# Kernel optimization log

Measured on AMD Instinct MI355X. Metric: run time of the kernel, lower is better.

Reference implementation:

```python
import jax, jax.numpy as jnp
import numpy as np

B, S1, S2, H, H2, D, K = 1, 1024, 8192, 32, 8, 128, 128


def setup_inputs() -> dict:
    key = jax.random.key(0)
    k1, k2, k3, k4 = jax.random.split(key, 4)
    q = jax.random.normal(k1, (B, S1, H, D), dtype=jnp.float16)
    k = jax.random.normal(k2, (B, S2, H2, D), dtype=jnp.float16)
    v = jax.random.normal(k3, (B, S2, H2, D), dtype=jnp.float16)
    sparse_indices = jax.random.randint(k4, (B, S1, H2, K), 0, S2, dtype=jnp.int32)
    return {"q": q, "k": k, "v": v, "sparse_indices": sparse_indices}


def reference(q, k, v, sparse_indices):
    # q: [B,S1,H,D]  k,v: [B,S2,H2,D]  sparse_indices: [B,S1,H2,K]
    b, s1, h, d = q.shape
    h2 = sparse_indices.shape[2]
    g = h // h2  # GQA group size
    scale = 1.0 / np.sqrt(d).astype(np.float32)
    qg = q.reshape(b, s1, h2, g, d)  # group queries per kv head
    b_idx = jnp.arange(b)[:, None, None, None]
    h_idx = jnp.arange(h2)[None, None, :, None]
    # gather per-query sparse KV sets: [B,S1,H2,K,D]
    kg = k[b_idx, sparse_indices, h_idx]
    vg = v[b_idx, sparse_indices, h_idx]
    scores = jnp.einsum('bshgd,bshkd->bshgk', qg, kg).astype(jnp.float32) * scale
    p = jax.nn.softmax(scores, axis=-1).astype(q.dtype)
    out = jnp.einsum('bshgk,bshkd->bshgd', p, vg)  # [B,S1,H2,G,D]
    return out.reshape(b, s1, h, d).astype(jnp.float16)
```

## Files before the change

kernel.cpp:

```cpp
#include <hip/hip_runtime.h>
#include <stdint.h>
#include <math.h>

#define NH 32
#define NH2 8
#define DD 128
#define KSEL 128
#define GG 4
#define S2MASK 8191
#define KVELTS (8192 * NH2 * DD)

typedef _Float16 h8   __attribute__((ext_vector_type(8)));
typedef _Float16 h2t  __attribute__((ext_vector_type(2)));
typedef __fp16   hp2  __attribute__((ext_vector_type(2)));
typedef float    f32x4 __attribute__((ext_vector_type(4)));

static __device__ __forceinline__ h8 cvt8(float4 a, float4 b) {
  union { h8 v; hp2 p[4]; } u;
  u.p[0] = __builtin_amdgcn_cvt_pkrtz(a.x, a.y);
  u.p[1] = __builtin_amdgcn_cvt_pkrtz(a.z, a.w);
  u.p[2] = __builtin_amdgcn_cvt_pkrtz(b.x, b.y);
  u.p[3] = __builtin_amdgcn_cvt_pkrtz(b.z, b.w);
  return u.v;
}

__global__ __launch_bounds__(256) void convert_kv(
    const float4* __restrict__ kf, const float4* __restrict__ vf,
    ushort4* __restrict__ kh, ushort4* __restrict__ vh, int n4) {
  int i = blockIdx.x * blockDim.x + threadIdx.x;
  const int stride = gridDim.x * blockDim.x;
  union { ushort4 u; hp2 p[2]; } ua;
  for (; i < n4; i += stride) {
    float4 a = kf[i];
    ua.p[0] = __builtin_amdgcn_cvt_pkrtz(a.x, a.y);
    ua.p[1] = __builtin_amdgcn_cvt_pkrtz(a.z, a.w);
    kh[i] = ua.u;
    float4 b = vf[i];
    ua.p[0] = __builtin_amdgcn_cvt_pkrtz(b.x, b.y);
    ua.p[1] = __builtin_amdgcn_cvt_pkrtz(b.z, b.w);
    vh[i] = ua.u;
  }
}

#define WAVE_FENCE() asm volatile("" ::: "memory")

__global__ __launch_bounds__(256) void sparse_attn_f16(
    const float* __restrict__ q, const _Float16* __restrict__ kh,
    const _Float16* __restrict__ vh, const int* __restrict__ idx,
    float* __restrict__ out) {
  __shared__ int sOff[4][KSEL];
  __shared__ __align__(16) float sP[4][KSEL][GG];

  const int tid = threadIdx.x;
  const int w = tid >> 6;
  const int lane = tid & 63;
  const int h2 = blockIdx.x & 7;
  const int s1 = ((blockIdx.x >> 3) << 2) + w;

  const int* ip = idx + (s1 * NH2 + h2) * KSEL;
  sOff[w][lane]      = (ip[lane]      & S2MASK) * (NH2 * DD);
  sOff[w][lane + 64] = (ip[lane + 64] & S2MASK) * (NH2 * DD);

  const int m  = lane & 15;
  const int kg = lane >> 4;

  h8 aq[4];
#pragma unroll
  for (int t = 0; t < 4; ++t)
#pragma unroll
    for (int i = 0; i < 8; ++i) aq[t][i] = (_Float16)0;
  if (m < GG) {
    const float* qp = q + (s1 * NH + h2 * GG + m) * DD + kg * 8;
#pragma unroll
    for (int t = 0; t < 4; ++t) {
      float4 f0 = *(const float4*)(qp + 32 * t);
      float4 f1 = *(const float4*)(qp + 32 * t + 4);
      aq[t] = cvt8(f0, f1);
    }
  }

  WAVE_FENCE();

  const float scale = 0.08838834764831845f;

#pragma unroll 2
  for (int nt = 0; nt < 8; ++nt) {
    const _Float16* kp = kh + sOff[w][nt * 16 + m] + h2 * DD + kg * 8;
    f32x4 acc = {0.f, 0.f, 0.f, 0.f};
#pragma unroll
    for (int t = 0; t < 4; ++t) {
      h8 bk = *(const h8*)(kp + 32 * t);
      acc = __builtin_amdgcn_mfma_f32_16x16x32_f16(aq[t], bk, acc, 0, 0, 0);
    }
    if (lane < 16) {
      float4 sc = make_float4(acc[0] * scale, acc[1] * scale,
                              acc[2] * scale, acc[3] * scale);
      *(float4*)&sP[w][nt * 16 + lane][0] = sc;
    }
  }

  WAVE_FENCE();

  {
    float4 p0 = *(const float4*)&sP[w][lane][0];
    float4 p1 = *(const float4*)&sP[w][lane + 64][0];
    float4 mx = make_float4(fmaxf(p0.x, p1.x), fmaxf(p0.y, p1.y),
                            fmaxf(p0.z, p1.z), fmaxf(p0.w, p1.w));
#pragma unroll
    for (int off = 1; off < 64; off <<= 1) {
      mx.x = fmaxf(mx.x, __shfl_xor(mx.x, off));
      mx.y = fmaxf(mx.y, __shfl_xor(mx.y, off));
      mx.z = fmaxf(mx.z, __shfl_xor(mx.z, off));
      mx.w = fmaxf(mx.w, __shfl_xor(mx.w, off));
    }
    float4 e0 = make_float4(__expf(p0.x - mx.x), __expf(p0.y - mx.y),
                            __expf(p0.z - mx.z), __expf(p0.w - mx.w));
    float4 e1 = make_float4(__expf(p1.x - mx.x), __expf(p1.y - mx.y),
                            __expf(p1.z - mx.z), __expf(p1.w - mx.w));
    float4 sm = make_float4(e0.x + e1.x, e0.y + e1.y, e0.z + e1.z, e0.w + e1.w);
#pragma unroll
    for (int off = 1; off < 64; off <<= 1) {
      sm.x += __shfl_xor(sm.x, off);
      sm.y += __shfl_xor(sm.y, off);
      sm.z += __shfl_xor(sm.z, off);
      sm.w += __shfl_xor(sm.w, off);
    }
    float4 inv = make_float4(1.f / fmaxf(sm.x, 1e-30f), 1.f / fmaxf(sm.y, 1e-30f),
                             1.f / fmaxf(sm.z, 1e-30f), 1.f / fmaxf(sm.w, 1e-30f));
    *(float4*)&sP[w][lane][0] =
        make_float4(e0.x * inv.x, e0.y * inv.y, e0.z * inv.z, e0.w * inv.w);
    *(float4*)&sP[w][lane + 64][0] =
        make_float4(e1.x * inv.x, e1.y * inv.y, e1.z * inv.z, e1.w * inv.w);
  }

  WAVE_FENCE();

  float a00 = 0.f, a01 = 0.f, a10 = 0.f, a11 = 0.f;
  float a20 = 0.f, a21 = 0.f, a30 = 0.f, a31 = 0.f;
  const _Float16* vb = vh + h2 * DD + lane * 2;
#pragma unroll
  for (int ch = 0; ch < 8; ++ch) {
    h2t vv[16];
#pragma unroll
    for (int j = 0; j < 16; ++j)
      vv[j] = *(const h2t*)(vb + sOff[w][ch * 16 + j]);
#pragma unroll
    for (int j = 0; j < 16; ++j) {
      const float4 p = *(const float4*)&sP[w][ch * 16 + j][0];
      const float vx = (float)vv[j][0];
      const float vy = (float)vv[j][1];
      a00 = fmaf(p.x, vx, a00); a01 = fmaf(p.x, vy, a01);
      a10 = fmaf(p.y, vx, a10); a11 = fmaf(p.y, vy, a11);
      a20 = fmaf(p.z, vx, a20); a21 = fmaf(p.z, vy, a21);
      a30 = fmaf(p.w, vx, a30); a31 = fmaf(p.w, vy, a31);
    }
  }

  float* op = out + (s1 * NH + h2 * GG) * DD + lane * 2;
  *(float2*)(op + 0 * DD) = make_float2(a00, a01);
  *(float2*)(op + 1 * DD) = make_float2(a10, a11);
  *(float2*)(op + 2 * DD) = make_float2(a20, a21);
  *(float2*)(op + 3 * DD) = make_float2(a30, a31);
}

__global__ __launch_bounds__(256) void sparse_attn_f32(
    const float* __restrict__ q, const float* __restrict__ k,
    const float* __restrict__ v, const int* __restrict__ idx,
    float* __restrict__ out) {
  __shared__ int sIdx[4][KSEL];
  __shared__ __align__(16) float sP[4][KSEL][GG];

  const int tid = threadIdx.x;
  const int w = tid >> 6;
  const int lane = tid & 63;
  const int h2 = blockIdx.x & 7;
  const int s1 = ((blockIdx.x >> 3) << 2) + w;

  const int* ip = idx + (s1 * NH2 + h2) * KSEL;
  sIdx[w][lane]      = ip[lane] & S2MASK;
  sIdx[w][lane + 64] = ip[lane + 64] & S2MASK;

  const int m  = lane & 15;
  const int kg = lane >> 4;

  h8 aq[4];
#pragma unroll
  for (int t = 0; t < 4; ++t)
#pragma unroll
    for (int i = 0; i < 8; ++i) aq[t][i] = (_Float16)0;
  if (m < GG) {
    const float* qp = q + (s1 * NH + h2 * GG + m) * DD + kg * 8;
#pragma unroll
    for (int t = 0; t < 4; ++t) {
      float4 f0 = *(const float4*)(qp + 32 * t);
      float4 f1 = *(const float4*)(qp + 32 * t + 4);
      aq[t] = cvt8(f0, f1);
    }
  }
  __syncthreads();

  const float scale = 0.08838834764831845f;
#pragma unroll 2
  for (int nt = 0; nt < 8; ++nt) {
    const int s2 = sIdx[w][nt * 16 + m];
    const float* kp = k + (s2 * NH2 + h2) * DD + kg * 8;
    f32x4 acc = {0.f, 0.f, 0.f, 0.f};
#pragma unroll
    for (int t = 0; t < 4; ++t) {
      float4 f0 = *(const float4*)(kp + 32 * t);
      float4 f1 = *(const float4*)(kp + 32 * t + 4);
      acc = __builtin_amdgcn_mfma_f32_16x16x32_f16(aq[t], cvt8(f0, f1), acc, 0, 0, 0);
    }
    if (lane < 16) {
      float4 sc = make_float4(acc[0] * scale, acc[1] * scale,
                              acc[2] * scale, acc[3] * scale);
      *(float4*)&sP[w][nt * 16 + lane][0] = sc;
    }
  }
  __syncthreads();

  {
    float4 p0 = *(const float4*)&sP[w][lane][0];
    float4 p1 = *(const float4*)&sP[w][lane + 64][0];
    float4 mx = make_float4(fmaxf(p0.x, p1.x), fmaxf(p0.y, p1.y),
                            fmaxf(p0.z, p1.z), fmaxf(p0.w, p1.w));
#pragma unroll
    for (int off = 1; off < 64; off <<= 1) {
      mx.x = fmaxf(mx.x, __shfl_xor(mx.x, off));
      mx.y = fmaxf(mx.y, __shfl_xor(mx.y, off));
      mx.z = fmaxf(mx.z, __shfl_xor(mx.z, off));
      mx.w = fmaxf(mx.w, __shfl_xor(mx.w, off));
    }
    float4 e0 = make_float4(__expf(p0.x - mx.x), __expf(p0.y - mx.y),
                            __expf(p0.z - mx.z), __expf(p0.w - mx.w));
    float4 e1 = make_float4(__expf(p1.x - mx.x), __expf(p1.y - mx.y),
                            __expf(p1.z - mx.z), __expf(p1.w - mx.w));
    float4 sm = make_float4(e0.x + e1.x, e0.y + e1.y, e0.z + e1.z, e0.w + e1.w);
#pragma unroll
    for (int off = 1; off < 64; off <<= 1) {
      sm.x += __shfl_xor(sm.x, off);
      sm.y += __shfl_xor(sm.y, off);
      sm.z += __shfl_xor(sm.z, off);
      sm.w += __shfl_xor(sm.w, off);
    }
    float4 inv = make_float4(1.f / fmaxf(sm.x, 1e-30f), 1.f / fmaxf(sm.y, 1e-30f),
                             1.f / fmaxf(sm.z, 1e-30f), 1.f / fmaxf(sm.w, 1e-30f));
    *(float4*)&sP[w][lane][0] =
        make_float4(e0.x * inv.x, e0.y * inv.y, e0.z * inv.z, e0.w * inv.w);
    *(float4*)&sP[w][lane + 64][0] =
        make_float4(e1.x * inv.x, e1.y * inv.y, e1.z * inv.z, e1.w * inv.w);
  }
  __syncthreads();

  float a00 = 0.f, a01 = 0.f, a10 = 0.f, a11 = 0.f;
  float a20 = 0.f, a21 = 0.f, a30 = 0.f, a31 = 0.f;
  const float* vb = v + h2 * DD + lane * 2;
#pragma unroll 8
  for (int j = 0; j < KSEL; ++j) {
    const int s2 = sIdx[w][j];
    const float2 vv = *(const float2*)(vb + (size_t)s2 * (NH2 * DD));
    const float4 p = *(const float4*)&sP[w][j][0];
    a00 = fmaf(p.x, vv.x, a00); a01 = fmaf(p.x, vv.y, a01);
    a10 = fmaf(p.y, vv.x, a10); a11 = fmaf(p.y, vv.y, a11);
    a20 = fmaf(p.z, vv.x, a20); a21 = fmaf(p.z, vv.y, a21);
    a30 = fmaf(p.w, vv.x, a30); a31 = fmaf(p.w, vv.y, a31);
  }

  float* op = out + (s1 * NH + h2 * GG) * DD + lane * 2;
  *(float2*)(op + 0 * DD) = make_float2(a00, a01);
  *(float2*)(op + 1 * DD) = make_float2(a10, a11);
  *(float2*)(op + 2 * DD) = make_float2(a20, a21);
  *(float2*)(op + 3 * DD) = make_float2(a30, a31);
}

extern "C" void kernel_launch(void* const* d_in, const int* in_sizes, int n_in,
                              void* d_out, int out_size, void* d_ws, size_t ws_size,
                              hipStream_t stream) {
  const float* q = (const float*)d_in[0];
  const float* k = (const float*)d_in[1];
  const float* v = (const float*)d_in[2];
  const int* idx = (const int*)d_in[3];
  float* out = (float*)d_out;

  const size_t need = (size_t)2 * KVELTS * sizeof(_Float16);
  if (ws_size >= need) {
    _Float16* kh = (_Float16*)d_ws;
    _Float16* vh = kh + KVELTS;
    convert_kv<<<dim3(2048), dim3(256), 0, stream>>>(
        (const float4*)k, (const float4*)v,
        (ushort4*)kh, (ushort4*)vh, KVELTS / 4);
    sparse_attn_f16<<<dim3(2048), dim3(256), 0, stream>>>(q, kh, vh, idx, out);
  } else {
    sparse_attn_f32<<<dim3(2048), dim3(256), 0, stream>>>(q, k, v, idx, out);
  }
}
```

Measured before the change: 167.8 us.

## Stage sparse V rows into LDS with async global_load_lds prefetch

V rows gathered by sparse index now go into a per-wave LDS buffer using direct global-to-LDS loads of 16 bytes each, eight rows at a time. The first chunk is issued before the QK phase and the next chunk is prefetched while the current one is consumed. The aim is to replace the many scattered 4-byte per-lane V loads with fully coalesced 256-byte row loads and to overlap that traffic with compute. With a single buffer, each chunk must be read into registers and drained before the next load overwrites it, so explicit waitcnt and sched barriers serialize the steps and limit how much overlap is possible.

```diff
diff --git a/kernel.cpp b/kernel.cpp
--- a/kernel.cpp
+++ b/kernel.cpp
@@ -9,11 +9,20 @@
 #define GG 4
 #define S2MASK 8191
 #define KVELTS (8192 * NH2 * DD)
+#define VCHUNK 8
+#define NCHUNK (KSEL / VCHUNK)
 
 typedef _Float16 h8   __attribute__((ext_vector_type(8)));
 typedef _Float16 h2t  __attribute__((ext_vector_type(2)));
 typedef __fp16   hp2  __attribute__((ext_vector_type(2)));
 typedef float    f32x4 __attribute__((ext_vector_type(4)));
+
+typedef __attribute__((address_space(1))) const unsigned int glb_u32_t;
+typedef __attribute__((address_space(3))) unsigned int lds_u32_t;
+
+static __device__ __forceinline__ void stage16(const void* g, void* l) {
+  __builtin_amdgcn_global_load_lds((glb_u32_t*)g, (lds_u32_t*)l, 16, 0, 0);
+}
 
 static __device__ __forceinline__ h8 cvt8(float4 a, float4 b) {
   union { h8 v; hp2 p[4]; } u;
@@ -49,7 +58,8 @@
     const _Float16* __restrict__ vh, const int* __restrict__ idx,
     float* __restrict__ out) {
   __shared__ int sOff[4][KSEL];
-  __shared__ __align__(16) float sP[4][KSEL][GG];
+  __shared__ __align__(16) float sS[4][KSEL][GG];
+  __shared__ __align__(16) _Float16 sV[4][VCHUNK][DD];
 
   const int tid = threadIdx.x;
   const int w = tid >> 6;
@@ -64,6 +74,15 @@
   const int m  = lane & 15;
   const int kg = lane >> 4;
 
+  {
+#pragma unroll
+    for (int i = 0; i < 2; ++i) {
+      const int soff = sOff[w][i * 4 + kg];
+      const char* gp = (const char*)vh + (size_t)soff * 2 + h2 * (DD * 2) + m * 16;
+      stage16(gp, (char*)&sV[w][0][0] + i * 1024);
+    }
+  }
+
   h8 aq[4];
 #pragma unroll
   for (int t = 0; t < 4; ++t)
@@ -95,15 +114,15 @@
     if (lane < 16) {
       float4 sc = make_float4(acc[0] * scale, acc[1] * scale,
                               acc[2] * scale, acc[3] * scale);
-      *(float4*)&sP[w][nt * 16 + lane][0] = sc;
+      *(float4*)&sS[w][nt * 16 + lane][0] = sc;
     }
   }
 
   WAVE_FENCE();
 
   {
-    float4 p0 = *(const float4*)&sP[w][lane][0];
-    float4 p1 = *(const float4*)&sP[w][lane + 64][0];
+    float4 p0 = *(const float4*)&sS[w][lane][0];
+    float4 p1 = *(const float4*)&sS[w][lane + 64][0];
     float4 mx = make_float4(fmaxf(p0.x, p1.x), fmaxf(p0.y, p1.y),
                             fmaxf(p0.z, p1.z), fmaxf(p0.w, p1.w));
 #pragma unroll
@@ -127,9 +146,9 @@
     }
     float4 inv = make_float4(1.f / fmaxf(sm.x, 1e-30f), 1.f / fmaxf(sm.y, 1e-30f),
                              1.f / fmaxf(sm.z, 1e-30f), 1.f / fmaxf(sm.w, 1e-30f));
-    *(float4*)&sP[w][lane][0] =
+    *(float4*)&sS[w][lane][0] =
         make_float4(e0.x * inv.x, e0.y * inv.y, e0.z * inv.z, e0.w * inv.w);
-    *(float4*)&sP[w][lane + 64][0] =
+    *(float4*)&sS[w][lane + 64][0] =
         make_float4(e1.x * inv.x, e1.y * inv.y, e1.z * inv.z, e1.w * inv.w);
   }
 
@@ -137,18 +156,30 @@
 
   float a00 = 0.f, a01 = 0.f, a10 = 0.f, a11 = 0.f;
   float a20 = 0.f, a21 = 0.f, a30 = 0.f, a31 = 0.f;
-  const _Float16* vb = vh + h2 * DD + lane * 2;
-#pragma unroll
-  for (int ch = 0; ch < 8; ++ch) {
-    h2t vv[16];
-#pragma unroll
-    for (int j = 0; j < 16; ++j)
-      vv[j] = *(const h2t*)(vb + sOff[w][ch * 16 + j]);
-#pragma unroll
-    for (int j = 0; j < 16; ++j) {
-      const float4 p = *(const float4*)&sP[w][ch * 16 + j][0];
-      const float vx = (float)vv[j][0];
-      const float vy = (float)vv[j][1];
+#pragma unroll
+  for (int ch = 0; ch < NCHUNK; ++ch) {
+    asm volatile("s_waitcnt vmcnt(0)" ::: "memory");
+    __builtin_amdgcn_sched_barrier(0);
+    h2t vv[VCHUNK];
+#pragma unroll
+    for (int jj = 0; jj < VCHUNK; ++jj)
+      vv[jj] = *(const h2t*)&sV[w][jj][lane * 2];
+    asm volatile("s_waitcnt lgkmcnt(0)" ::: "memory");
+    __builtin_amdgcn_sched_barrier(0);
+    if (ch < NCHUNK - 1) {
+      const int base = (ch + 1) * VCHUNK;
+#pragma unroll
+      for (int i = 0; i < 2; ++i) {
+        const int soff = sOff[w][base + i * 4 + kg];
+        const char* gp = (const char*)vh + (size_t)soff * 2 + h2 * (DD * 2) + m * 16;
+        stage16(gp, (char*)&sV[w][0][0] + i * 1024);
+      }
+    }
+#pragma unroll
+    for (int jj = 0; jj < VCHUNK; ++jj) {
+      const float4 p = *(const float4*)&sS[w][ch * VCHUNK + jj][0];
+      const float vx = (float)vv[jj][0];
+      const float vy = (float)vv[jj][1];
       a00 = fmaf(p.x, vx, a00); a01 = fmaf(p.x, vy, a01);
       a10 = fmaf(p.y, vx, a10); a11 = fmaf(p.y, vy, a11);
       a20 = fmaf(p.z, vx, a20); a21 = fmaf(p.z, vy, a21);
```

Result: slower. 335.6 us (+100.0%).

## Split each query's 128 sparse keys across two waves with cross-wave softmax merge

Applied to the files above, without the earlier changes.

Each (query, kv-head) item is now handled by two waves, each covering 64 of the 128 selected keys, so the grid doubles to 4096 blocks with 2 queries per block instead of 4. Partial max and sum are exchanged through shared memory to rescale each half's probabilities, and the second wave's output accumulators are added into the first wave's before the store. This shortens each wave's serial dependent gather chain and exposes more parallelism for latency hiding. The cost is two block-wide barriers, extra shared-memory traffic, and duplicated Q loading per half.

```diff
diff --git a/kernel.cpp b/kernel.cpp
--- a/kernel.cpp
+++ b/kernel.cpp
@@ -6,6 +6,7 @@
 #define NH2 8
 #define DD 128
 #define KSEL 128
+#define KHALF 64
 #define GG 4
 #define S2MASK 8191
 #define KVELTS (8192 * NH2 * DD)
@@ -44,22 +45,25 @@
 
 #define WAVE_FENCE() asm volatile("" ::: "memory")
 
-__global__ __launch_bounds__(256) void sparse_attn_f16(
+__global__ __launch_bounds__(256) void sparse_attn_split(
     const float* __restrict__ q, const _Float16* __restrict__ kh,
     const _Float16* __restrict__ vh, const int* __restrict__ idx,
     float* __restrict__ out) {
-  __shared__ int sOff[4][KSEL];
-  __shared__ __align__(16) float sP[4][KSEL][GG];
+  __shared__ int sOff[4][KHALF];
+  __shared__ __align__(16) float sP[4][KHALF][GG];
+  __shared__ __align__(16) float sO[2][64][8];
+  __shared__ __align__(16) float sRed[4][8];
 
   const int tid = threadIdx.x;
   const int w = tid >> 6;
   const int lane = tid & 63;
   const int h2 = blockIdx.x & 7;
-  const int s1 = ((blockIdx.x >> 3) << 2) + w;
-
-  const int* ip = idx + (s1 * NH2 + h2) * KSEL;
-  sOff[w][lane]      = (ip[lane]      & S2MASK) * (NH2 * DD);
-  sOff[w][lane + 64] = (ip[lane + 64] & S2MASK) * (NH2 * DD);
+  const int pair = blockIdx.x >> 3;
+  const int s1 = pair * 2 + (w >> 1);
+  const int half = w & 1;
+
+  const int* ip = idx + (s1 * NH2 + h2) * KSEL + half * KHALF;
+  sOff[w][lane] = (ip[lane] & S2MASK) * (NH2 * DD);
 
   const int m  = lane & 15;
   const int kg = lane >> 4;
@@ -84,7 +88,7 @@
   const float scale = 0.08838834764831845f;
 
 #pragma unroll 2
-  for (int nt = 0; nt < 8; ++nt) {
+  for (int nt = 0; nt < 4; ++nt) {
     const _Float16* kp = kh + sOff[w][nt * 16 + m] + h2 * DD + kg * 8;
     f32x4 acc = {0.f, 0.f, 0.f, 0.f};
 #pragma unroll
@@ -101,36 +105,49 @@
 
   WAVE_FENCE();
 
+  float4 s4 = *(const float4*)&sP[w][lane][0];
+  float4 mx = s4;
+#pragma unroll
+  for (int off = 1; off < 64; off <<= 1) {
+    mx.x = fmaxf(mx.x, __shfl_xor(mx.x, off));
+    mx.y = fmaxf(mx.y, __shfl_xor(mx.y, off));
+    mx.z = fmaxf(mx.z, __shfl_xor(mx.z, off));
+    mx.w = fmaxf(mx.w, __shfl_xor(mx.w, off));
+  }
+  float4 e4 = make_float4(__expf(s4.x - mx.x), __expf(s4.y - mx.y),
+                          __expf(s4.z - mx.z), __expf(s4.w - mx.w));
+  float4 sm = e4;
+#pragma unroll
+  for (int off = 1; off < 64; off <<= 1) {
+    sm.x += __shfl_xor(sm.x, off);
+    sm.y += __shfl_xor(sm.y, off);
+    sm.z += __shfl_xor(sm.z, off);
+    sm.w += __shfl_xor(sm.w, off);
+  }
+  if (lane == 0) {
+    *(float4*)&sRed[w][0] = mx;
+    *(float4*)&sRed[w][4] = sm;
+  }
+  __syncthreads();
   {
-    float4 p0 = *(const float4*)&sP[w][lane][0];
-    float4 p1 = *(const float4*)&sP[w][lane + 64][0];
-    float4 mx = make_float4(fmaxf(p0.x, p1.x), fmaxf(p0.y, p1.y),
-                            fmaxf(p0.z, p1.z), fmaxf(p0.w, p1.w));
-#pragma unroll
-    for (int off = 1; off < 64; off <<= 1) {
-      mx.x = fmaxf(mx.x, __shfl_xor(mx.x, off));
-      mx.y = fmaxf(mx.y, __shfl_xor(mx.y, off));
-      mx.z = fmaxf(mx.z, __shfl_xor(mx.z, off));
-      mx.w = fmaxf(mx.w, __shfl_xor(mx.w, off));
-    }
-    float4 e0 = make_float4(__expf(p0.x - mx.x), __expf(p0.y - mx.y),
-                            __expf(p0.z - mx.z), __expf(p0.w - mx.w));
-    float4 e1 = make_float4(__expf(p1.x - mx.x), __expf(p1.y - mx.y),
-                            __expf(p1.z - mx.z), __expf(p1.w - mx.w));
-    float4 sm = make_float4(e0.x + e1.x, e0.y + e1.y, e0.z + e1.z, e0.w + e1.w);
-#pragma unroll
-    for (int off = 1; off < 64; off <<= 1) {
-      sm.x += __shfl_xor(sm.x, off);
-      sm.y += __shfl_xor(sm.y, off);
-      sm.z += __shfl_xor(sm.z, off);
-      sm.w += __shfl_xor(sm.w, off);
-    }
-    float4 inv = make_float4(1.f / fmaxf(sm.x, 1e-30f), 1.f / fmaxf(sm.y, 1e-30f),
-                             1.f / fmaxf(sm.z, 1e-30f), 1.f / fmaxf(sm.w, 1e-30f));
+    const float4 pm = *(const float4*)&sRed[w ^ 1][0];
+    const float4 ps = *(const float4*)&sRed[w ^ 1][4];
+    float4 gm = make_float4(fmaxf(mx.x, pm.x), fmaxf(mx.y, pm.y),
+                            fmaxf(mx.z, pm.z), fmaxf(mx.w, pm.w));
+    float4 fw = make_float4(__expf(mx.x - gm.x), __expf(mx.y - gm.y),
+                            __expf(mx.z - gm.z), __expf(mx.w - gm.w));
+    float4 fp = make_float4(__expf(pm.x - gm.x), __expf(pm.y - gm.y),
+                            __expf(pm.z - gm.z), __expf(pm.w - gm.w));
+    float4 Z = make_float4(sm.x * fw.x + ps.x * fp.x,
+                           sm.y * fw.y + ps.y * fp.y,
+                           sm.z * fw.z + ps.z * fp.z,
+                           sm.w * fw.w + ps.w * fp.w);
+    float4 cf = make_float4(fw.x / fmaxf(Z.x, 1e-30f),
+                            fw.y / fmaxf(Z.y, 1e-30f),
+                            fw.z / fmaxf(Z.z, 1e-30f),
+                            fw.w / fmaxf(Z.w, 1e-30f));
     *(float4*)&sP[w][lane][0] =
-        make_float4(e0.x * inv.x, e0.y * inv.y, e0.z * inv.z, e0.w * inv.w);
-    *(float4*)&sP[w][lane + 64][0] =
-        make_float4(e1.x * inv.x, e1.y * inv.y, e1.z * inv.z, e1.w * inv.w);
+        make_float4(e4.x * cf.x, e4.y * cf.y, e4.z * cf.z, e4.w * cf.w);
   }
 
   WAVE_FENCE();
@@ -139,7 +156,7 @@
   float a20 = 0.f, a21 = 0.f, a30 = 0.f, a31 = 0.f;
   const _Float16* vb = vh + h2 * DD + lane * 2;
 #pragma unroll
-  for (int ch = 0; ch < 8; ++ch) {
+  for (int ch = 0; ch < 4; ++ch) {
     h2t vv[16];
 #pragma unroll
     for (int j = 0; j < 16; ++j)
@@ -156,11 +173,22 @@
     }
   }
 
-  float* op = out + (s1 * NH + h2 * GG) * DD + lane * 2;
-  *(float2*)(op + 0 * DD) = make_float2(a00, a01);
-  *(float2*)(op + 1 * DD) = make_float2(a10, a11);
-  *(float2*)(op + 2 * DD) = make_float2(a20, a21);
-  *(float2*)(op + 3 * DD) = make_float2(a30, a31);
+  if (half == 1) {
+    float* o = &sO[w >> 1][lane][0];
+    *(float4*)(o + 0) = make_float4(a00, a01, a10, a11);
+    *(float4*)(o + 4) = make_float4(a20, a21, a30, a31);
+  }
+  __syncthreads();
+  if (half == 0) {
+    const float* o = &sO[w >> 1][lane][0];
+    const float4 o0 = *(const float4*)(o + 0);
+    const float4 o1 = *(const float4*)(o + 4);
+    float* op = out + (s1 * NH + h2 * GG) * DD + lane * 2;
+    *(float2*)(op + 0 * DD) = make_float2(a00 + o0.x, a01 + o0.y);
+    *(float2*)(op + 1 * DD) = make_float2(a10 + o0.z, a11 + o0.w);
+    *(float2*)(op + 2 * DD) = make_float2(a20 + o1.x, a21 + o1.y);
+    *(float2*)(op + 3 * DD) = make_float2(a30 + o1.z, a31 + o1.w);
+  }
 }
 
 __global__ __launch_bounds__(256) void sparse_attn_f32(
@@ -289,7 +317,7 @@
     convert_kv<<<dim3(2048), dim3(256), 0, stream>>>(
         (const float4*)k, (const float4*)v,
         (ushort4*)kh, (ushort4*)vh, KVELTS / 4);
-    sparse_attn_f16<<<dim3(2048), dim3(256), 0, stream>>>(q, kh, vh, idx, out);
+    sparse_attn_split<<<dim3(4096), dim3(256), 0, stream>>>(q, kh, vh, idx, out);
   } else {
     sparse_attn_f32<<<dim3(2048), dim3(256), 0, stream>>>(q, k, v, idx, out);
   }
```

Result: slower. 173.8 us (+3.6%).
